# Optimization experiments

Hardware: AMD Instinct MI355X
Metric: run time of the kernel (lower is better)

Reference implementation:

```python
import jax, jax.numpy as jnp
import numpy as np

E, T, H, I, K = 16, 2048, 1024, 512, 2  # experts, tokens, hidden, intermediate, top_k


def setup_inputs() -> dict:
    key = jax.random.key(0)
    k1, k2, k3, k4, k5 = jax.random.split(key, 5)
    hidden_states = jax.random.normal(k1, (T, H), dtype=jnp.float32)
    topk_weights = jax.random.uniform(k2, (T, K), dtype=jnp.float32)
    topk_indices = jax.random.randint(k3, (T, K), 0, E, dtype=jnp.int32)
    # learned expert params, viewed per expert as in _view_experts_weight()
    gate_up_proj = jax.random.normal(k4, (E, H, 2 * I), dtype=jnp.float32) * 0.02
    down_proj = jax.random.normal(k5, (E, I, H), dtype=jnp.float32) * 0.02
    return {
        "hidden_states": hidden_states,
        "topk_weights": topk_weights,
        "topk_indices": topk_indices,
        "gate_up_proj": gate_up_proj,
        "down_proj": down_proj,
    }


def reference(hidden_states, topk_weights, topk_indices, gate_up_proj, down_proj):
    """MoE experts: per-expert gate_up GEMM -> silu-gate -> down GEMM,
    combined with top-k routing weights (index_add over tokens in the original).

    Equivalent dense formulation: combine[e, t] = sum_k topk_weights[t, k] * [topk_indices[t, k] == e];
    out = sum_e expert_e(hidden_states) * combine[e][:, None]. Tokens not routed to e get
    weight 0, matching the original gather/scatter-add exactly (including duplicate
    expert ids within a token, which accumulate).
    """
    num_experts = gate_up_proj.shape[0]
    one_hot = jax.nn.one_hot(topk_indices, num_experts, dtype=topk_weights.dtype)  # [T, K, E]
    combine = jnp.einsum("tk,tke->et", topk_weights, one_hot)  # [E, T]

    def body(acc, xs):
        w_gu, w_d, w = xs  # [H, 2I], [I, H], [T]
        gate_up = hidden_states @ w_gu  # [T, 2I]
        gate, up = jnp.split(gate_up, 2, axis=-1)
        expert_out = (jax.nn.silu(gate) * up) @ w_d  # [T, H]
        return acc + expert_out * w[:, None], None

    init = jnp.zeros_like(hidden_states)
    out, _ = jax.lax.scan(body, init, (gate_up_proj, down_proj, combine))
    return out.astype(hidden_states.dtype)
```

## Files before the change

kernel.cpp:

```cpp
#include <hip/hip_runtime.h>

#define E_ 16
#define T_ 2048
#define H_ 1024
#define I_ 512
#define NPAIR 4096
#define BM 128
#define MAXTILE 48

typedef __bf16 bf16x8 __attribute__((ext_vector_type(8)));
typedef float  f32x4  __attribute__((ext_vector_type(4)));

static __device__ __forceinline__ unsigned short f2bf(float f) {
    __bf16 h = (__bf16)f;
    return __builtin_bit_cast(unsigned short, h);
}

static __device__ __forceinline__ void gl_lds16(const void* g, void* l) {
    __builtin_amdgcn_global_load_lds(
        (const __attribute__((address_space(1))) unsigned int*)g,
        (__attribute__((address_space(3))) unsigned int*)l,
        16, 0, 0);
}

__global__ __launch_bounds__(256) void route_kernel(
    const float* __restrict__ tw, const int* __restrict__ ti,
    int* __restrict__ offs, int* __restrict__ tile_e, int* __restrict__ tile_r,
    int* __restrict__ pair_ts, float* __restrict__ pair_w, int* __restrict__ inv)
{
    __shared__ unsigned short hist[256][E_];
    __shared__ int ebase[E_];
    const int tid = threadIdx.x;

    int e_loc[16];
    unsigned short h[E_];
    for (int e = 0; e < E_; ++e) h[e] = 0;
    for (int i = 0; i < 16; ++i) {
        int p = tid * 16 + i;
        int e = ti[p];
        e_loc[i] = e;
        h[e]++;
    }
    for (int e = 0; e < E_; ++e) hist[tid][e] = h[e];
    __syncthreads();

    if (tid < E_) {
        int e = tid, run = 0;
        for (int t = 0; t < 256; ++t) {
            unsigned short c = hist[t][e];
            hist[t][e] = (unsigned short)run;
            run += c;
        }
        ebase[e] = run;
    }
    __syncthreads();
    if (tid == 0) {
        int run = 0, nt = 0;
        for (int e = 0; e < E_; ++e) {
            int c = ebase[e];
            offs[e] = run; ebase[e] = run;
            for (int r = 0; r < c; r += BM) { tile_e[nt] = e; tile_r[nt] = r; ++nt; }
            run += c;
        }
        offs[E_] = run;
        for (; nt < MAXTILE; ++nt) tile_e[nt] = -1;
    }
    __syncthreads();

    int cur[E_];
    for (int e = 0; e < E_; ++e) cur[e] = ebase[e] + hist[tid][e];
    for (int i = 0; i < 16; ++i) {
        int p = tid * 16 + i;
        int e = e_loc[i];
        int pos = cur[e]++;
        pair_ts[pos] = p;
        pair_w[pos]  = tw[p];
        inv[p]       = pos;
    }
}

__global__ __launch_bounds__(256) void gather_kernel(
    const float* __restrict__ X, const int* __restrict__ pair_ts,
    unsigned short* __restrict__ Ag)
{
    const int q = blockIdx.x;
    const int t = pair_ts[q] >> 1;
    const int c = threadIdx.x * 4;
    const float4 x = *(const float4*)&X[(size_t)t * H_ + c];
    ushort4 b; b.x = f2bf(x.x); b.y = f2bf(x.y); b.z = f2bf(x.z); b.w = f2bf(x.w);
    *(ushort4*)&Ag[(size_t)q * H_ + c] = b;
}

__global__ __launch_bounds__(256) void transform_kernel(
    const float* __restrict__ W1, const float* __restrict__ W2,
    unsigned short* __restrict__ W1t, unsigned short* __restrict__ W2t)
{
    __shared__ unsigned short tile[64][140];
    const int t   = threadIdx.x;
    const int bid = blockIdx.x;

    const float* src;
    unsigned short* dstO;
    int isW1, ch, ks, e;
    if (bid < 2048) {
        isW1 = 1;
        ch = bid & 7; ks = (bid >> 3) & 15; e = bid >> 7;
        src  = W1 + (size_t)e * (H_ * 2 * I_) + (size_t)(ks * 64) * 1024 + ch * 128;
        dstO = W1t;
    } else {
        int b2 = bid - 2048;
        isW1 = 0;
        ch = b2 & 7; ks = (b2 >> 3) & 7; e = b2 >> 6;
        src  = W2 + (size_t)e * (I_ * H_) + (size_t)(ks * 64) * 1024 + ch * 128;
        dstO = W2t;
    }

    const int r0 = t >> 5, c4 = (t & 31) * 4;
    #pragma unroll
    for (int i = 0; i < 8; ++i) {
        const float4 v = *(const float4*)(src + (size_t)(r0 + i * 8) * 1024 + c4);
        ushort4 u;
        u.x = f2bf(v.x); u.y = f2bf(v.y); u.z = f2bf(v.z); u.w = f2bf(v.w);
        *(ushort4*)&tile[r0 + i * 8][c4] = u;
    }
    __syncthreads();

    const int cl = t >> 1;
    const int c  = ch * 128 + cl;
    int bn_; size_t dstoff;
    if (isW1) {
        int half = c >> 9, cc = c & 511;
        int cb = cc >> 5, grp = (cc >> 4) & 1, sub = cc & 15;
        bn_ = grp * 32 + half * 16 + sub;
        dstoff = ((size_t)((e * 16 + cb) * 16 + ks)) * 4096;
    } else {
        int hb = c >> 6; bn_ = c & 63;
        dstoff = ((size_t)((e * 16 + hb) * 8 + ks)) * 4096;
    }
    unsigned short* dp = dstO + dstoff + bn_ * 64;
    #pragma unroll
    for (int u = 0; u < 4; ++u) {
        int p  = (t & 1) * 4 + u;
        int kl = (p ^ (bn_ & 7)) * 8;
        union { unsigned short us[8]; uint4 q; } g_;
        #pragma unroll
        for (int j = 0; j < 8; ++j) g_.us[j] = tile[kl + j][cl];
        *(uint4*)&dp[p * 8] = g_.q;
    }
}

#define MFMA_TILE(AS, BS)                                                              \
    _Pragma("unroll")                                                                  \
    for (int kkj = 0; kkj < 2; ++kkj) {                                                \
        const int j0 = kkj * 4;                                                        \
        bf16x8 af[4], bfr[2];                                                          \
        _Pragma("unroll")                                                              \
        for (int m = 0; m < 4; ++m)                                                    \
            af[m] = *(const bf16x8*)&AS[wm * 64 + m * 16 + lrow][((j0 + lk) ^ (lrow & 7)) * 8]; \
        _Pragma("unroll")                                                              \
        for (int n = 0; n < 2; ++n)                                                    \
            bfr[n] = *(const bf16x8*)&BS[wn * 32 + n * 16 + lrow][((j0 + lk) ^ (lrow & 7)) * 8]; \
        _Pragma("unroll")                                                              \
        for (int m = 0; m < 4; ++m)                                                    \
            _Pragma("unroll")                                                          \
            for (int n = 0; n < 2; ++n)                                                \
                acc[m][n] = __builtin_amdgcn_mfma_f32_16x16x32_bf16(af[m], bfr[n], acc[m][n], 0, 0, 0); \
    }

#define STAGE_A(BUF, KB)                                                               \
    _Pragma("unroll")                                                                  \
    for (int i = 0; i < 4; ++i) gl_lds16(asrc[i] + (KB), &As[BUF][w * 32 + i * 8][0]);

#define STAGE_B(BUF, KS)                                                               \
    _Pragma("unroll")                                                                  \
    for (int i = 0; i < 2; ++i)                                                        \
        gl_lds16(bsrcB + (size_t)(KS) * 4096 + i * 512,                                \
                 &Bs[BUF][0][0] + w * 1024 + i * 512);

#define K_PIPE(NT)                                                                     \
    STAGE_A(0, 0)                                                                      \
    STAGE_B(0, 0)                                                                      \
    __syncthreads();                                                                   \
    int cur = 0;                                                                       \
    _Pragma("unroll")                                                                  \
    for (int kt = 0; kt < (NT); ++kt) {                                                \
        int nxt = cur ^ 1;                                                             \
        if (kt + 1 < (NT)) { STAGE_A(nxt, (kt + 1) * 64) STAGE_B(nxt, kt + 1) }        \
        __builtin_amdgcn_s_setprio(1);                                                 \
        MFMA_TILE(As[cur], Bs[cur])                                                    \
        __builtin_amdgcn_s_setprio(0);                                                 \
        __syncthreads();                                                               \
        cur = nxt;                                                                     \
    }

__global__ __launch_bounds__(256, 3) void gemm1_kernel(
    const unsigned short* __restrict__ Ag, const unsigned short* __restrict__ W1t,
    const int* __restrict__ offs, const int* __restrict__ tile_e,
    const int* __restrict__ tile_r, unsigned short* __restrict__ act)
{
    const int e = tile_e[blockIdx.y];
    if (e < 0) return;
    const int rbeg = offs[e], rend = offs[e + 1];
    const int ne   = rend - rbeg;
    const int row0 = tile_r[blockIdx.y];
    const int cb   = blockIdx.x;
    const int c0   = cb * 32;

    __shared__ unsigned short As[2][128][64];
    __shared__ unsigned short Bs[2][64][64];

    const int tid  = threadIdx.x;
    const int lane = tid & 63;
    const int w    = tid >> 6;
    const int wm   = w >> 1, wn = w & 1;
    const int lrow = lane & 15;
    const int lk   = lane >> 4;

    const int r8 = lane >> 3, gr = lane & 7;
    const unsigned short* asrc[4];
    #pragma unroll
    for (int i = 0; i < 4; ++i) {
        int q = rbeg + row0 + w * 32 + i * 8 + r8;
        if (q > rend - 1) q = rend - 1;
        asrc[i] = Ag + (size_t)q * H_ + (gr ^ r8) * 8;
    }

    const unsigned short* bsrcB =
        W1t + ((size_t)(e * 16 + cb) * 16) * 4096 + w * 1024 + lane * 8;

    f32x4 acc[4][2];
    #pragma unroll
    for (int m = 0; m < 4; ++m)
        #pragma unroll
        for (int n = 0; n < 2; ++n)
            acc[m][n] = f32x4{0.f, 0.f, 0.f, 0.f};

    K_PIPE(16)

    for (int m = 0; m < 4; ++m) {
        #pragma unroll
        for (int reg = 0; reg < 4; ++reg) {
            int rloc = wm * 64 + m * 16 + lk * 4 + reg;
            if (row0 + rloc < ne) {
                int q = rbeg + row0 + rloc;
                float g = acc[m][0][reg], u = acc[m][1][reg];
                float a = g / (1.f + __expf(-g)) * u;
                act[(size_t)q * I_ + c0 + wn * 16 + lrow] = f2bf(a);
            }
        }
    }
}

__global__ __launch_bounds__(256, 3) void gemm2_kernel(
    const unsigned short* __restrict__ Agact, const unsigned short* __restrict__ W2t,
    const int* __restrict__ offs, const int* __restrict__ tile_e,
    const int* __restrict__ tile_r, const float* __restrict__ pair_w,
    float* __restrict__ C2)
{
    const int e = tile_e[blockIdx.y];
    if (e < 0) return;
    const int rbeg = offs[e], rend = offs[e + 1];
    const int ne   = rend - rbeg;
    const int row0 = tile_r[blockIdx.y];
    const int hb   = blockIdx.x;
    const int c0   = hb * 64;

    __shared__ unsigned short As[2][128][64];
    __shared__ unsigned short Bs[2][64][64];

    const int tid  = threadIdx.x;
    const int lane = tid & 63;
    const int w    = tid >> 6;
    const int wm   = w >> 1, wn = w & 1;
    const int lrow = lane & 15;
    const int lk   = lane >> 4;

    const int r8 = lane >> 3, gr = lane & 7;
    const unsigned short* asrc[4];
    #pragma unroll
    for (int i = 0; i < 4; ++i) {
        int q = rbeg + row0 + w * 32 + i * 8 + r8;
        if (q > rend - 1) q = rend - 1;
        asrc[i] = Agact + (size_t)q * I_ + (gr ^ r8) * 8;
    }

    const unsigned short* bsrcB =
        W2t + ((size_t)(e * 16 + hb) * 8) * 4096 + w * 1024 + lane * 8;

    f32x4 acc[4][2];
    #pragma unroll
    for (int m = 0; m < 4; ++m)
        #pragma unroll
        for (int n = 0; n < 2; ++n)
            acc[m][n] = f32x4{0.f, 0.f, 0.f, 0.f};

    K_PIPE(8)

    for (int m = 0; m < 4; ++m) {
        #pragma unroll
        for (int reg = 0; reg < 4; ++reg) {
            int rloc = wm * 64 + m * 16 + lk * 4 + reg;
            if (row0 + rloc < ne) {
                int q   = rbeg + row0 + rloc;
                float wt = pair_w[q];
                #pragma unroll
                for (int n = 0; n < 2; ++n) {
                    int cg = c0 + wn * 32 + n * 16 + lrow;
                    C2[(size_t)q * H_ + cg] = wt * acc[m][n][reg];
                }
            }
        }
    }
}

__global__ __launch_bounds__(256) void combine_kernel(
    const float* __restrict__ C2, const int* __restrict__ inv,
    float* __restrict__ out)
{
    const int t = blockIdx.x;
    const int c = threadIdx.x * 4;
    const int q0 = inv[2 * t], q1 = inv[2 * t + 1];
    const float4 a = *(const float4*)&C2[(size_t)q0 * H_ + c];
    const float4 b = *(const float4*)&C2[(size_t)q1 * H_ + c];
    float4 o;
    o.x = a.x + b.x; o.y = a.y + b.y; o.z = a.z + b.z; o.w = a.w + b.w;
    *(float4*)&out[(size_t)t * H_ + c] = o;
}

extern "C" void kernel_launch(void* const* d_in, const int* in_sizes, int n_in,
                              void* d_out, int out_size, void* d_ws, size_t ws_size,
                              hipStream_t stream)
{
    const float* X  = (const float*)d_in[0];
    const float* tw = (const float*)d_in[1];
    const int*   ti = (const int*)d_in[2];
    const float* W1 = (const float*)d_in[3];
    const float* W2 = (const float*)d_in[4];
    float* out = (float*)d_out;

    char* ws = (char*)d_ws;
    int*   offs    = (int*)(ws);
    int*   tile_e  = (int*)(ws + 128);
    int*   tile_r  = (int*)(ws + 320);
    int*   pair_ts = (int*)(ws + 1024);
    float* pair_w  = (float*)(ws + 1024 + NPAIR * 4);
    int*   inv     = (int*)(ws + 1024 + NPAIR * 8);
    unsigned short* Ag  = (unsigned short*)(ws + (size_t)(1u << 16));
    unsigned short* act = (unsigned short*)(ws + (size_t)(1u << 16) + 8388608);
    unsigned short* W1t = (unsigned short*)(ws + (size_t)(1u << 16) + 12582912);
    unsigned short* W2t = (unsigned short*)(ws + (size_t)(1u << 16) + 46137344);
    float*          C2  = (float*)(ws + (size_t)(1u << 16) + 62914560);

    transform_kernel<<<3072, 256, 0, stream>>>(W1, W2, W1t, W2t);

    route_kernel<<<1, 256, 0, stream>>>(tw, ti, offs, tile_e, tile_r, pair_ts, pair_w, inv);

    gather_kernel<<<NPAIR, 256, 0, stream>>>(X, pair_ts, Ag);

    gemm1_kernel<<<dim3(16, MAXTILE), 256, 0, stream>>>(Ag, W1t, offs, tile_e, tile_r, act);

    gemm2_kernel<<<dim3(16, MAXTILE), 256, 0, stream>>>(act, W2t, offs, tile_e, tile_r, pair_w, C2);

    combine_kernel<<<T_, 256, 0, stream>>>(C2, inv, out);
}
```

Baseline: 89.74 us.

## Fuse prep kernels, gather rows inside GEMM1, scatter GEMM2 output atomically

The weight transform, routing and X-to-bf16 conversion are merged into one prep kernel launch. The gathered copy of X per pair is dropped: X is converted once per token and GEMM1 indexes rows through pair_ts. GEMM2 now atomically adds weighted results straight into the output, which is zeroed by a memset, so the C2 buffer and the combine kernel go away. This saves kernel launches and the traffic of the intermediate buffers, at the cost of scattered atomic float adds and summation order that depends on scheduling.

```diff
diff --git a/kernel.cpp b/kernel.cpp
--- a/kernel.cpp
+++ b/kernel.cpp
@@ -23,129 +23,129 @@
         16, 0, 0);
 }
 
-__global__ __launch_bounds__(256) void route_kernel(
-    const float* __restrict__ tw, const int* __restrict__ ti,
+__global__ __launch_bounds__(256) void prep_kernel(
+    const float* __restrict__ W1, const float* __restrict__ W2,
+    const float* __restrict__ X,  const float* __restrict__ tw,
+    const int* __restrict__ ti,
+    unsigned short* __restrict__ W1t, unsigned short* __restrict__ W2t,
+    unsigned short* __restrict__ Agc,
     int* __restrict__ offs, int* __restrict__ tile_e, int* __restrict__ tile_r,
-    int* __restrict__ pair_ts, float* __restrict__ pair_w, int* __restrict__ inv)
+    int* __restrict__ pair_ts, float* __restrict__ pair_w)
 {
-    __shared__ unsigned short hist[256][E_];
+    __shared__ unsigned short tw_s[4][16][130];
     __shared__ int ebase[E_];
     const int tid = threadIdx.x;
-
-    int e_loc[16];
-    unsigned short h[E_];
-    for (int e = 0; e < E_; ++e) h[e] = 0;
-    for (int i = 0; i < 16; ++i) {
-        int p = tid * 16 + i;
-        int e = ti[p];
-        e_loc[i] = e;
-        h[e]++;
-    }
-    for (int e = 0; e < E_; ++e) hist[tid][e] = h[e];
-    __syncthreads();
-
-    if (tid < E_) {
-        int e = tid, run = 0;
-        for (int t = 0; t < 256; ++t) {
-            unsigned short c = hist[t][e];
-            hist[t][e] = (unsigned short)run;
-            run += c;
-        }
-        ebase[e] = run;
-    }
-    __syncthreads();
-    if (tid == 0) {
-        int run = 0, nt = 0;
-        for (int e = 0; e < E_; ++e) {
-            int c = ebase[e];
-            offs[e] = run; ebase[e] = run;
-            for (int r = 0; r < c; r += BM) { tile_e[nt] = e; tile_r[nt] = r; ++nt; }
-            run += c;
-        }
-        offs[E_] = run;
-        for (; nt < MAXTILE; ++nt) tile_e[nt] = -1;
-    }
-    __syncthreads();
-
-    int cur[E_];
-    for (int e = 0; e < E_; ++e) cur[e] = ebase[e] + hist[tid][e];
-    for (int i = 0; i < 16; ++i) {
-        int p = tid * 16 + i;
-        int e = e_loc[i];
-        int pos = cur[e]++;
-        pair_ts[pos] = p;
-        pair_w[pos]  = tw[p];
-        inv[p]       = pos;
-    }
-}
-
-__global__ __launch_bounds__(256) void gather_kernel(
-    const float* __restrict__ X, const int* __restrict__ pair_ts,
-    unsigned short* __restrict__ Ag)
-{
-    const int q = blockIdx.x;
-    const int t = pair_ts[q] >> 1;
-    const int c = threadIdx.x * 4;
-    const float4 x = *(const float4*)&X[(size_t)t * H_ + c];
-    ushort4 b; b.x = f2bf(x.x); b.y = f2bf(x.y); b.z = f2bf(x.z); b.w = f2bf(x.w);
-    *(ushort4*)&Ag[(size_t)q * H_ + c] = b;
-}
-
-__global__ __launch_bounds__(256) void transform_kernel(
-    const float* __restrict__ W1, const float* __restrict__ W2,
-    unsigned short* __restrict__ W1t, unsigned short* __restrict__ W2t)
-{
-    __shared__ unsigned short tile[64][140];
-    const int t   = threadIdx.x;
     const int bid = blockIdx.x;
 
-    const float* src;
-    unsigned short* dstO;
-    int isW1, ch, ks, e;
-    if (bid < 2048) {
-        isW1 = 1;
-        ch = bid & 7; ks = (bid >> 3) & 15; e = bid >> 7;
-        src  = W1 + (size_t)e * (H_ * 2 * I_) + (size_t)(ks * 64) * 1024 + ch * 128;
-        dstO = W1t;
+    if (bid < 3072) {
+        const float* src;
+        unsigned short* dstO;
+        int isW1, ch, ks, e;
+        if (bid < 2048) {
+            isW1 = 1;
+            ch = bid & 7; ks = (bid >> 3) & 15; e = bid >> 7;
+            src  = W1 + (size_t)e * (H_ * 2 * I_) + (size_t)(ks * 64) * 1024 + ch * 128;
+            dstO = W1t;
+        } else {
+            int b2 = bid - 2048;
+            isW1 = 0;
+            ch = b2 & 7; ks = (b2 >> 3) & 7; e = b2 >> 6;
+            src  = W2 + (size_t)e * (I_ * H_) + (size_t)(ks * 64) * 1024 + ch * 128;
+            dstO = W2t;
+        }
+        const int w    = tid >> 6;
+        const int lane = tid & 63;
+
+        float4 r[8];
+        #pragma unroll
+        for (int i = 0; i < 8; ++i) {
+            int row = 16 * w + i * 2 + (lane >> 5);
+            r[i] = *(const float4*)(src + (size_t)row * 1024 + (lane & 31) * 4);
+        }
+        #pragma unroll
+        for (int i = 0; i < 8; ++i) {
+            ushort4 u;
+            u.x = f2bf(r[i].x); u.y = f2bf(r[i].y); u.z = f2bf(r[i].z); u.w = f2bf(r[i].w);
+            *(ushort4*)&tw_s[w][i * 2 + (lane >> 5)][(lane & 31) * 4] = u;
+        }
+        #pragma unroll
+        for (int ci = 0; ci < 2; ++ci) {
+            const int cl = 2 * lane + ci;
+            const int c  = ch * 128 + cl;
+            int bn_; size_t dstoff;
+            if (isW1) {
+                int half = c >> 9, cc = c & 511;
+                int cb = cc >> 5, grp = (cc >> 4) & 1, sub = cc & 15;
+                bn_ = grp * 32 + half * 16 + sub;
+                dstoff = ((size_t)((e * 16 + cb) * 16 + ks)) * 4096;
+            } else {
+                int hb = c >> 6; bn_ = c & 63;
+                dstoff = ((size_t)((e * 16 + hb) * 8 + ks)) * 4096;
+            }
+            unsigned short* dp = dstO + dstoff + bn_ * 64;
+            #pragma unroll
+            for (int s = 0; s < 2; ++s) {
+                int band = 2 * w + s;
+                int p    = band ^ (bn_ & 7);
+                union { unsigned short us[8]; uint4 q; } g_;
+                #pragma unroll
+                for (int j = 0; j < 8; ++j) g_.us[j] = tw_s[w][s * 8 + j][cl];
+                *(uint4*)&dp[p * 8] = g_.q;
+            }
+        }
+    } else if (bid == 3072) {
+        unsigned short (*hist)[E_] = (unsigned short (*)[E_])&tw_s[0][0][0];
+        int e_loc[16];
+        unsigned short h[E_];
+        for (int e = 0; e < E_; ++e) h[e] = 0;
+        for (int i = 0; i < 16; ++i) {
+            int p = tid * 16 + i;
+            int e = ti[p];
+            e_loc[i] = e;
+            h[e]++;
+        }
+        for (int e = 0; e < E_; ++e) hist[tid][e] = h[e];
+        __syncthreads();
+        if (tid < E_) {
+            int e = tid, run = 0;
+            for (int t = 0; t < 256; ++t) {
+                unsigned short c = hist[t][e];
+                hist[t][e] = (unsigned short)run;
+                run += c;
+            }
+            ebase[e] = run;
+        }
+        __syncthreads();
+        if (tid == 0) {
+            int run = 0, nt = 0;
+            for (int e = 0; e < E_; ++e) {
+                int c = ebase[e];
+                offs[e] = run; ebase[e] = run;
+                for (int r = 0; r < c; r += BM) { tile_e[nt] = e; tile_r[nt] = r; ++nt; }
+                run += c;
+            }
+            offs[E_] = run;
+            for (; nt < MAXTILE; ++nt) tile_e[nt] = -1;
+        }
+        __syncthreads();
+        int cur[E_];
+        for (int e = 0; e < E_; ++e) cur[e] = ebase[e] + hist[tid][e];
+        for (int i = 0; i < 16; ++i) {
+            int p = tid * 16 + i;
+            int e = e_loc[i];
+            int pos = cur[e]++;
+            pair_ts[pos] = p;
+            pair_w[pos]  = tw[p];
+        }
     } else {
-        int b2 = bid - 2048;
-        isW1 = 0;
-        ch = b2 & 7; ks = (b2 >> 3) & 7; e = b2 >> 6;
-        src  = W2 + (size_t)e * (I_ * H_) + (size_t)(ks * 64) * 1024 + ch * 128;
-        dstO = W2t;
-    }
-
-    const int r0 = t >> 5, c4 = (t & 31) * 4;
-    #pragma unroll
-    for (int i = 0; i < 8; ++i) {
-        const float4 v = *(const float4*)(src + (size_t)(r0 + i * 8) * 1024 + c4);
-        ushort4 u;
-        u.x = f2bf(v.x); u.y = f2bf(v.y); u.z = f2bf(v.z); u.w = f2bf(v.w);
-        *(ushort4*)&tile[r0 + i * 8][c4] = u;
-    }
-    __syncthreads();
-
-    const int cl = t >> 1;
-    const int c  = ch * 128 + cl;
-    int bn_; size_t dstoff;
-    if (isW1) {
-        int half = c >> 9, cc = c & 511;
-        int cb = cc >> 5, grp = (cc >> 4) & 1, sub = cc & 15;
-        bn_ = grp * 32 + half * 16 + sub;
-        dstoff = ((size_t)((e * 16 + cb) * 16 + ks)) * 4096;
-    } else {
-        int hb = c >> 6; bn_ = c & 63;
-        dstoff = ((size_t)((e * 16 + hb) * 8 + ks)) * 4096;
-    }
-    unsigned short* dp = dstO + dstoff + bn_ * 64;
-    #pragma unroll
-    for (int u = 0; u < 4; ++u) {
-        int p  = (t & 1) * 4 + u;
-        int kl = (p ^ (bn_ & 7)) * 8;
-        union { unsigned short us[8]; uint4 q; } g_;
-        #pragma unroll
-        for (int j = 0; j < 8; ++j) g_.us[j] = tile[kl + j][cl];
-        *(uint4*)&dp[p * 8] = g_.q;
+        const int rb = (bid - 3073) * 16;
+        const int c  = tid * 4;
+        #pragma unroll
+        for (int i = 0; i < 16; ++i) {
+            const float4 x = *(const float4*)&X[(size_t)(rb + i) * H_ + c];
+            ushort4 b; b.x = f2bf(x.x); b.y = f2bf(x.y); b.z = f2bf(x.z); b.w = f2bf(x.w);
+            *(ushort4*)&Agc[(size_t)(rb + i) * H_ + c] = b;
+        }
     }
 }
 
@@ -194,9 +194,10 @@
     }
 
 __global__ __launch_bounds__(256, 3) void gemm1_kernel(
-    const unsigned short* __restrict__ Ag, const unsigned short* __restrict__ W1t,
+    const unsigned short* __restrict__ Agc, const unsigned short* __restrict__ W1t,
     const int* __restrict__ offs, const int* __restrict__ tile_e,
-    const int* __restrict__ tile_r, unsigned short* __restrict__ act)
+    const int* __restrict__ tile_r, const int* __restrict__ pair_ts,
+    unsigned short* __restrict__ act)
 {
     const int e = tile_e[blockIdx.y];
     if (e < 0) return;
@@ -222,7 +223,8 @@
     for (int i = 0; i < 4; ++i) {
         int q = rbeg + row0 + w * 32 + i * 8 + r8;
         if (q > rend - 1) q = rend - 1;
-        asrc[i] = Ag + (size_t)q * H_ + (gr ^ r8) * 8;
+        int tok = pair_ts[q] >> 1;
+        asrc[i] = Agc + (size_t)tok * H_ + (gr ^ r8) * 8;
     }
 
     const unsigned short* bsrcB =
@@ -252,10 +254,10 @@
 }
 
 __global__ __launch_bounds__(256, 3) void gemm2_kernel(
-    const unsigned short* __restrict__ Agact, const unsigned short* __restrict__ W2t,
+    const unsigned short* __restrict__ act, const unsigned short* __restrict__ W2t,
     const int* __restrict__ offs, const int* __restrict__ tile_e,
-    const int* __restrict__ tile_r, const float* __restrict__ pair_w,
-    float* __restrict__ C2)
+    const int* __restrict__ tile_r, const int* __restrict__ pair_ts,
+    const float* __restrict__ pair_w, float* __restrict__ out)
 {
     const int e = tile_e[blockIdx.y];
     if (e < 0) return;
@@ -281,7 +283,7 @@
     for (int i = 0; i < 4; ++i) {
         int q = rbeg + row0 + w * 32 + i * 8 + r8;
         if (q > rend - 1) q = rend - 1;
-        asrc[i] = Agact + (size_t)q * I_ + (gr ^ r8) * 8;
+        asrc[i] = act + (size_t)q * I_ + (gr ^ r8) * 8;
     }
 
     const unsigned short* bsrcB =
@@ -302,29 +304,16 @@
             int rloc = wm * 64 + m * 16 + lk * 4 + reg;
             if (row0 + rloc < ne) {
                 int q   = rbeg + row0 + rloc;
+                int tok = pair_ts[q] >> 1;
                 float wt = pair_w[q];
                 #pragma unroll
                 for (int n = 0; n < 2; ++n) {
                     int cg = c0 + wn * 32 + n * 16 + lrow;
-                    C2[(size_t)q * H_ + cg] = wt * acc[m][n][reg];
+                    atomicAdd(&out[(size_t)tok * H_ + cg], wt * acc[m][n][reg]);
                 }
             }
         }
     }
-}
-
-__global__ __launch_bounds__(256) void combine_kernel(
-    const float* __restrict__ C2, const int* __restrict__ inv,
-    float* __restrict__ out)
-{
-    const int t = blockIdx.x;
-    const int c = threadIdx.x * 4;
-    const int q0 = inv[2 * t], q1 = inv[2 * t + 1];
-    const float4 a = *(const float4*)&C2[(size_t)q0 * H_ + c];
-    const float4 b = *(const float4*)&C2[(size_t)q1 * H_ + c];
-    float4 o;
-    o.x = a.x + b.x; o.y = a.y + b.y; o.z = a.z + b.z; o.w = a.w + b.w;
-    *(float4*)&out[(size_t)t * H_ + c] = o;
 }
 
 extern "C" void kernel_launch(void* const* d_in, const int* in_sizes, int n_in,
@@ -344,22 +333,17 @@
     int*   tile_r  = (int*)(ws + 320);
     int*   pair_ts = (int*)(ws + 1024);
     float* pair_w  = (float*)(ws + 1024 + NPAIR * 4);
-    int*   inv     = (int*)(ws + 1024 + NPAIR * 8);
-    unsigned short* Ag  = (unsigned short*)(ws + (size_t)(1u << 16));
-    unsigned short* act = (unsigned short*)(ws + (size_t)(1u << 16) + 8388608);
-    unsigned short* W1t = (unsigned short*)(ws + (size_t)(1u << 16) + 12582912);
-    unsigned short* W2t = (unsigned short*)(ws + (size_t)(1u << 16) + 46137344);
-    float*          C2  = (float*)(ws + (size_t)(1u << 16) + 62914560);
-
-    transform_kernel<<<3072, 256, 0, stream>>>(W1, W2, W1t, W2t);
-
-    route_kernel<<<1, 256, 0, stream>>>(tw, ti, offs, tile_e, tile_r, pair_ts, pair_w, inv);
-
-    gather_kernel<<<NPAIR, 256, 0, stream>>>(X, pair_ts, Ag);
-
-    gemm1_kernel<<<dim3(16, MAXTILE), 256, 0, stream>>>(Ag, W1t, offs, tile_e, tile_r, act);
-
-    gemm2_kernel<<<dim3(16, MAXTILE), 256, 0, stream>>>(act, W2t, offs, tile_e, tile_r, pair_w, C2);
-
-    combine_kernel<<<T_, 256, 0, stream>>>(C2, inv, out);
-}
+    unsigned short* Agc = (unsigned short*)(ws + (size_t)(1u << 16));
+    unsigned short* act = (unsigned short*)(ws + (size_t)(1u << 16) + 4194304);
+    unsigned short* W1t = (unsigned short*)(ws + (size_t)(1u << 16) + 8388608);
+    unsigned short* W2t = (unsigned short*)(ws + (size_t)(1u << 16) + 41943040);
+
+    hipMemsetAsync(d_out, 0, (size_t)out_size * sizeof(float), stream);
+
+    prep_kernel<<<3201, 256, 0, stream>>>(W1, W2, X, tw, ti, W1t, W2t, Agc,
+                                          offs, tile_e, tile_r, pair_ts, pair_w);
+
+    gemm1_kernel<<<dim3(16, MAXTILE), 256, 0, stream>>>(Agc, W1t, offs, tile_e, tile_r, pair_ts, act);
+
+    gemm2_kernel<<<dim3(16, MAXTILE), 256, 0, stream>>>(act, W2t, offs, tile_e, tile_r, pair_ts, pair_w, out);
+}
```

Result: faster. 84.89 us (-5.4%).
